# Optimization experiments

Measured on AMD Instinct MI355X. Metric: run time of the kernel, lower is better.

The kernel has to match this reference:

```python
import jax, jax.numpy as jnp
import numpy as np

B = 4096
IN_FEATS = 1024
OUT_FEATS = 1024
NUM_HEADS = 16
NUM_MEMS = 4096
HEAD_DIM = OUT_FEATS // NUM_HEADS
TEMPERATURE = 1.0
EPS = 0.0  # original code uses plain jnp.linalg.norm (no eps)


def setup_inputs() -> dict:
    key = jax.random.key(0)
    k1, k2, k3 = jax.random.split(key, 3)
    x = jax.random.normal(k1, (B, IN_FEATS), dtype=jnp.float32)
    # eqx.nn.Linear stores weight as [out, in]; uniform-like init replaced with normal scaled
    W_q = jax.random.normal(k2, (OUT_FEATS, IN_FEATS), dtype=jnp.float32) * (1.0 / np.sqrt(IN_FEATS))
    memories = jax.random.normal(k3, (NUM_HEADS, NUM_MEMS, HEAD_DIM), dtype=jnp.float32) * 0.02
    return {"x": x, "W_q": W_q, "memories": memories}


def reference(x, W_q, memories):
    # q = query_proj(x): [B, out_feats] -> [B, H, d]
    q = (x @ W_q.T).reshape(B, NUM_HEADS, HEAD_DIM)
    # L2-normalize queries and memories along feature dim
    q_norm = q / jnp.linalg.norm(q, axis=-1, keepdims=True)
    mem_norm = memories / jnp.linalg.norm(memories, axis=-1, keepdims=True)
    # cosine-similarity scores: [B, H, M]
    attn_scores = jnp.einsum('bhd,hmd->bhm', q_norm, mem_norm)
    # soft readout (hard=False branch)
    mem_probs = jax.nn.softmax(attn_scores / TEMPERATURE, axis=-1)
    # weighted combine of normalized memories, scaled by sqrt(head_dim)
    out = jnp.einsum('bhm,hmd->bhd', mem_probs, mem_norm) * jnp.sqrt(HEAD_DIM).astype(x.dtype)
    return out.reshape(B, OUT_FEATS)
```

## Files before the change

kernel.cpp:

```cpp
#include <hip/hip_runtime.h>
#include <stdint.h>

#define B_SZ  4096
#define HEADS 16
#define HD    64
#define M_SZ  4096
#define K_IN  1024
#define SW    72
#define LOG2E 1.44269504088896f

typedef _Float16 f16;
typedef f16  f16x4 __attribute__((ext_vector_type(4)));
typedef f16  f16x8 __attribute__((ext_vector_type(8)));
typedef float f32x4 __attribute__((ext_vector_type(4)));

union U8 { uint4 u4; f16x8 h8; unsigned int ui[4]; unsigned short us[8]; };

__device__ __forceinline__ unsigned short f2h(float f) {
    _Float16 h = (_Float16)f;
    return __builtin_bit_cast(unsigned short, h);
}
__device__ __forceinline__ f16x8 ldsv8(const unsigned short* p) {
    U8 u; u.u4 = *reinterpret_cast<const uint4*>(p); return u.h8;
}

#if __has_builtin(__builtin_amdgcn_exp2f)
#define EXP2F(x) __builtin_amdgcn_exp2f(x)
#else
#define EXP2F(x) __expf((x) * 0.6931471805599453f)
#endif

__device__ __forceinline__ void gload_lds16(const void* g, void* l) {
    __builtin_amdgcn_global_load_lds(
        (const __attribute__((address_space(1))) void*)g,
        (__attribute__((address_space(3))) void*)l, 16, 0, 0);
}

__global__ __launch_bounds__(256) void k_conv(const float* __restrict__ x,
                                              const float* __restrict__ Wq,
                                              unsigned short* __restrict__ xh,
                                              unsigned short* __restrict__ Wh) {
    const int b = blockIdx.x;
    const float* src;
    unsigned short* dst;
    size_t base;
    if (b < 2048) { src = x;  dst = xh; base = (size_t)b * 2048; }
    else          { src = Wq; dst = Wh; base = (size_t)(b - 2048) * 2048; }
    const size_t i = base + (size_t)threadIdx.x * 8;
    float4 f0 = reinterpret_cast<const float4*>(src + i)[0];
    float4 f1 = reinterpret_cast<const float4*>(src + i)[1];
    U8 u;
    u.us[0] = f2h(f0.x); u.us[1] = f2h(f0.y); u.us[2] = f2h(f0.z); u.us[3] = f2h(f0.w);
    u.us[4] = f2h(f1.x); u.us[5] = f2h(f1.y); u.us[6] = f2h(f1.z); u.us[7] = f2h(f1.w);
    *reinterpret_cast<uint4*>(dst + i) = u.u4;
}

__global__ __launch_bounds__(256) void k_prep_mem(const float* __restrict__ mem,
                                                  unsigned short* __restrict__ F) {
    __shared__ float part[64][4];
    __shared__ float scale[64];
    __shared__ unsigned short Tn[64 * SW];

    const int h  = blockIdx.y;
    const int tl = blockIdx.x;
    const int m0 = tl * 64;
    const int tid = threadIdx.x;
    const int r = tid >> 2;
    const int c = tid & 3;

    const float* src = mem + ((size_t)(h * M_SZ + m0 + r)) * HD + c * 16;
    float v[16];
    float ss = 0.f;
#pragma unroll
    for (int i = 0; i < 4; i++) {
        float4 f = reinterpret_cast<const float4*>(src)[i];
        v[4*i+0] = f.x; v[4*i+1] = f.y; v[4*i+2] = f.z; v[4*i+3] = f.w;
        ss += f.x*f.x + f.y*f.y + f.z*f.z + f.w*f.w;
    }
    part[r][c] = ss;
    __syncthreads();
    if (tid < 64) {
        float s = part[tid][0] + part[tid][1] + part[tid][2] + part[tid][3];
        scale[tid] = rsqrtf(s);
    }
    __syncthreads();
    const float sc = scale[r];

    U8 a, b;
#pragma unroll
    for (int i = 0; i < 8; i++) { a.us[i] = f2h(v[i] * sc); b.us[i] = f2h(v[8 + i] * sc); }
    *reinterpret_cast<uint4*>(&Tn[r * SW + c * 16])     = a.u4;
    *reinterpret_cast<uint4*>(&Tn[r * SW + c * 16 + 8]) = b.u4;
    __syncthreads();

    const int w = tid >> 6, lane = tid & 63;
    const int l15 = lane & 15, quad = lane >> 4;
    unsigned short* Fd = F + ((size_t)(h * 64 + tl) * 16) * 512;

#pragma unroll
    for (int i = 0; i < 2; i++) {
        const int ch = w * 2 + i, g = ch >> 1, s = ch & 1;
        const int mp = 32 * (g >> 1) + ((l15 >> 2) * 8) + 4 * (g & 1) + (l15 & 3);
        uint4 vv = *reinterpret_cast<const uint4*>(&Tn[mp * SW + s * 32 + quad * 8]);
        *reinterpret_cast<uint4*>(Fd + ch * 512 + lane * 8) = vv;
    }
#pragma unroll
    for (int i = 0; i < 2; i++) {
        const int c2 = w * 2 + i, p = c2 >> 2, n = c2 & 3;
        U8 u;
#pragma unroll
        for (int j = 0; j < 8; j++)
            u.us[j] = Tn[(32 * p + quad * 8 + j) * SW + n * 16 + l15];
        *reinterpret_cast<uint4*>(Fd + (8 + c2) * 512 + lane * 8) = u.u4;
    }
}

__global__ __launch_bounds__(256, 2) void k_qproj(const unsigned short* __restrict__ xh,
                                                  const unsigned short* __restrict__ Wh,
                                                  unsigned short* __restrict__ qn) {
    __shared__ unsigned short As[128 * SW];
    __shared__ unsigned short Bs[64 * SW];

    const int b0 = blockIdx.x * 128;
    const int n0 = blockIdx.y * 64;
    const int t = threadIdx.x;
    const int w = t >> 6, lane = t & 63;
    const int l15 = lane & 15, quad = lane >> 4;

    f32x4 acc[2][4] = {};

    for (int kb = 0; kb < K_IN; kb += 64) {
        __syncthreads();
        {
            const unsigned short* px = xh + (size_t)(b0 + (t >> 1)) * K_IN + kb + (t & 1) * 32;
            const unsigned short* pw = Wh + (size_t)(n0 + (t >> 2)) * K_IN + kb + (t & 3) * 16;
            uint4 av[4];
#pragma unroll
            for (int i = 0; i < 4; i++) av[i] = reinterpret_cast<const uint4*>(px)[i];
            uint4 bv[2];
#pragma unroll
            for (int i = 0; i < 2; i++) bv[i] = reinterpret_cast<const uint4*>(pw)[i];
#pragma unroll
            for (int i = 0; i < 4; i++)
                *reinterpret_cast<uint4*>(&As[(t >> 1) * SW + (t & 1) * 32 + i * 8]) = av[i];
#pragma unroll
            for (int i = 0; i < 2; i++)
                *reinterpret_cast<uint4*>(&Bs[(t >> 2) * SW + (t & 3) * 16 + i * 8]) = bv[i];
        }
        __syncthreads();

#pragma unroll
        for (int s = 0; s < 2; s++) {
            f16x8 af[2];
#pragma unroll
            for (int qg = 0; qg < 2; qg++)
                af[qg] = ldsv8(&As[(w * 32 + qg * 16 + l15) * SW + s * 32 + quad * 8]);
#pragma unroll
            for (int g = 0; g < 4; g++) {
                f16x8 bf_ = ldsv8(&Bs[(g * 16 + l15) * SW + s * 32 + quad * 8]);
#pragma unroll
                for (int qg = 0; qg < 2; qg++)
                    acc[qg][g] = __builtin_amdgcn_mfma_f32_16x16x32_f16(af[qg], bf_, acc[qg][g], 0, 0, 0);
            }
        }
    }

    __syncthreads();
    unsigned short* Ct = As;
#pragma unroll
    for (int qg = 0; qg < 2; qg++) {
        float ssq[4];
#pragma unroll
        for (int r = 0; r < 4; r++) {
            float s = 0.f;
#pragma unroll
            for (int g = 0; g < 4; g++) s += acc[qg][g][r] * acc[qg][g][r];
            ssq[r] = s;
        }
#pragma unroll
        for (int mask = 1; mask <= 8; mask <<= 1)
#pragma unroll
            for (int r = 0; r < 4; r++) ssq[r] += __shfl_xor(ssq[r], mask, 64);
#pragma unroll
        for (int r = 0; r < 4; r++) {
            float inv = rsqrtf(ssq[r]) * LOG2E;
#pragma unroll
            for (int g = 0; g < 4; g++)
                Ct[(w * 32 + qg * 16 + quad * 4 + r) * SW + g * 16 + l15] = f2h(acc[qg][g][r] * inv);
        }
    }
    __syncthreads();

    const int row = t >> 1, half = (t & 1) * 32;
    unsigned short* dq = qn + (size_t)(b0 + row) * 1024 + n0 + half;
#pragma unroll
    for (int i = 0; i < 4; i++)
        reinterpret_cast<uint4*>(dq)[i] = *reinterpret_cast<const uint4*>(&Ct[row * SW + half + i * 8]);
}

__global__ __launch_bounds__(512, 4) void k_attn(const unsigned short* __restrict__ qn,
                                                 const unsigned short* __restrict__ F,
                                                 float* __restrict__ out) {
    __shared__ unsigned short buf[2][8192];

    const int b = blockIdx.x;
    const int h  = 2 * (b & 7) + (b >> 8);
    const int b0 = ((b >> 3) & 31) * 128;
    const int t = threadIdx.x;
    const int w = t >> 6, lane = t & 63;
    const int l15 = lane & 15, quad = lane >> 4;

    f16x8 qf[2];
#pragma unroll
    for (int s = 0; s < 2; s++) {
        U8 u;
        u.u4 = *reinterpret_cast<const uint4*>(
            qn + (size_t)(b0 + w * 16 + l15) * 1024 + h * 64 + s * 32 + quad * 8);
        qf[s] = u.h8;
    }

    const unsigned short* Fh = F + (size_t)h * 64 * 8192;

    f32x4 accO[4] = {};
    float lsum = 0.f;

    f16x8 puA[2], puB[2];
    f16x8 bwA[8], bwB[8];

#pragma unroll
    for (int i = 0; i < 2; i++) {
        const int ch = w * 2 + i;
        gload_lds16(Fh + ch * 512 + lane * 8, &buf[0][ch * 512]);
    }
    __syncthreads();
    {
        f16x8 am[8];
#pragma unroll
        for (int ch = 0; ch < 8; ch++) am[ch] = ldsv8(&buf[0][ch * 512 + lane * 8]);
#pragma unroll
        for (int ch = 0; ch < 8; ch++) bwA[ch] = ldsv8(&buf[0][(8 + ch) * 512 + lane * 8]);
#pragma unroll
        for (int i = 0; i < 2; i++) {
            const int ch = w * 2 + i;
            gload_lds16(Fh + 8192 + ch * 512 + lane * 8, &buf[1][ch * 512]);
        }
#pragma unroll
        for (int p = 0; p < 2; p++) {
            f32x4 t0 = {0.f,0.f,0.f,0.f}, t1 = {0.f,0.f,0.f,0.f};
            t0 = __builtin_amdgcn_mfma_f32_16x16x32_f16(am[4*p+0], qf[0], t0, 0, 0, 0);
            t0 = __builtin_amdgcn_mfma_f32_16x16x32_f16(am[4*p+1], qf[1], t0, 0, 0, 0);
            t1 = __builtin_amdgcn_mfma_f32_16x16x32_f16(am[4*p+2], qf[0], t1, 0, 0, 0);
            t1 = __builtin_amdgcn_mfma_f32_16x16x32_f16(am[4*p+3], qf[1], t1, 0, 0, 0);
            float p0 = EXP2F(t0[0]), p1 = EXP2F(t0[1]), p2 = EXP2F(t0[2]), p3 = EXP2F(t0[3]);
            float p4 = EXP2F(t1[0]), p5 = EXP2F(t1[1]), p6 = EXP2F(t1[2]), p7 = EXP2F(t1[3]);
            lsum += ((p0 + p1) + (p2 + p3)) + ((p4 + p5) + (p6 + p7));
            U8 pu;
#if __has_builtin(__builtin_amdgcn_cvt_pkrtz)
            pu.ui[0] = __builtin_bit_cast(unsigned int, __builtin_amdgcn_cvt_pkrtz(p0, p1));
            pu.ui[1] = __builtin_bit_cast(unsigned int, __builtin_amdgcn_cvt_pkrtz(p2, p3));
            pu.ui[2] = __builtin_bit_cast(unsigned int, __builtin_amdgcn_cvt_pkrtz(p4, p5));
            pu.ui[3] = __builtin_bit_cast(unsigned int, __builtin_amdgcn_cvt_pkrtz(p6, p7));
#else
            pu.us[0]=f2h(p0); pu.us[1]=f2h(p1); pu.us[2]=f2h(p2); pu.us[3]=f2h(p3);
            pu.us[4]=f2h(p4); pu.us[5]=f2h(p5); pu.us[6]=f2h(p6); pu.us[7]=f2h(p7);
#endif
            puA[p] = pu.h8;
        }
    }

    auto body = [&](int tl, f16x8 (&puC)[2], f16x8 (&bwC)[8],
                            f16x8 (&puN)[2], f16x8 (&bwN)[8]) {
        __syncthreads();
        const unsigned short* lb = buf[(tl + 1) & 1];
        f16x8 amn[8];
#pragma unroll
        for (int ch = 0; ch < 8; ch++) amn[ch] = ldsv8(&lb[ch * 512 + lane * 8]);
#pragma unroll
        for (int ch = 0; ch < 8; ch++) bwN[ch] = ldsv8(&lb[(8 + ch) * 512 + lane * 8]);
        if (tl + 2 < 64) {
            const unsigned short* gsrc = Fh + (size_t)(tl + 2) * 8192;
#pragma unroll
            for (int i = 0; i < 2; i++) {
                const int ch = w * 2 + i;
                gload_lds16(gsrc + ch * 512 + lane * 8, &buf[tl & 1][ch * 512]);
            }
        }

        f32x4 sa[2], sb[2];
        auto expPack = [&](int p) {
            float p0 = EXP2F(sa[p][0]), p1 = EXP2F(sa[p][1]), p2 = EXP2F(sa[p][2]), p3 = EXP2F(sa[p][3]);
            float p4 = EXP2F(sb[p][0]), p5 = EXP2F(sb[p][1]), p6 = EXP2F(sb[p][2]), p7 = EXP2F(sb[p][3]);
            lsum += ((p0 + p1) + (p2 + p3)) + ((p4 + p5) + (p6 + p7));
            U8 pu;
#if __has_builtin(__builtin_amdgcn_cvt_pkrtz)
            pu.ui[0] = __builtin_bit_cast(unsigned int, __builtin_amdgcn_cvt_pkrtz(p0, p1));
            pu.ui[1] = __builtin_bit_cast(unsigned int, __builtin_amdgcn_cvt_pkrtz(p2, p3));
            pu.ui[2] = __builtin_bit_cast(unsigned int, __builtin_amdgcn_cvt_pkrtz(p4, p5));
            pu.ui[3] = __builtin_bit_cast(unsigned int, __builtin_amdgcn_cvt_pkrtz(p6, p7));
#else
            pu.us[0]=f2h(p0); pu.us[1]=f2h(p1); pu.us[2]=f2h(p2); pu.us[3]=f2h(p3);
            pu.us[4]=f2h(p4); pu.us[5]=f2h(p5); pu.us[6]=f2h(p6); pu.us[7]=f2h(p7);
#endif
            puN[p] = pu.h8;
        };

#pragma unroll
        for (int p = 0; p < 2; p++) {
            f32x4 t0 = {0.f,0.f,0.f,0.f}, t1 = {0.f,0.f,0.f,0.f};
            t0 = __builtin_amdgcn_mfma_f32_16x16x32_f16(amn[4*p+0], qf[0], t0, 0, 0, 0);
            t0 = __builtin_amdgcn_mfma_f32_16x16x32_f16(amn[4*p+1], qf[1], t0, 0, 0, 0);
            t1 = __builtin_amdgcn_mfma_f32_16x16x32_f16(amn[4*p+2], qf[0], t1, 0, 0, 0);
            t1 = __builtin_amdgcn_mfma_f32_16x16x32_f16(amn[4*p+3], qf[1], t1, 0, 0, 0);
            sa[p] = t0; sb[p] = t1;
#pragma unroll
            for (int n = 0; n < 4; n++)
                accO[n] = __builtin_amdgcn_mfma_f32_16x16x32_f16(puC[p], bwC[p * 4 + n], accO[n], 0, 0, 0);
            if (p >= 1) expPack(p - 1);
        }
        expPack(1);
    };

    for (int tt = 0; tt < 31; ++tt) {
        body(2 * tt,     puA, bwA, puB, bwB);
        body(2 * tt + 1, puB, bwB, puA, bwA);
    }
    body(62, puA, bwA, puB, bwB);

#pragma unroll
    for (int p = 0; p < 2; p++) {
#pragma unroll
        for (int n = 0; n < 4; n++)
            accO[n] = __builtin_amdgcn_mfma_f32_16x16x32_f16(puB[p], bwB[p * 4 + n], accO[n], 0, 0, 0);
    }

    {
        float s = lsum;
        s += __shfl_xor(s, 16, 64);
        s += __shfl_xor(s, 32, 64);
        float inv = 8.0f / s;
#pragma unroll
        for (int r = 0; r < 4; r++) {
            float iv = __shfl(inv, quad * 4 + r, 64);
            float* po = out + (size_t)(b0 + w * 16 + quad * 4 + r) * 1024 + h * 64;
#pragma unroll
            for (int n = 0; n < 4; n++)
                po[n * 16 + l15] = accO[n][r] * iv;
        }
    }
}

extern "C" void kernel_launch(void* const* d_in, const int* in_sizes, int n_in,
                              void* d_out, int out_size, void* d_ws, size_t ws_size,
                              hipStream_t stream) {
    (void)in_sizes; (void)n_in; (void)out_size; (void)ws_size;
    const float* x   = (const float*)d_in[0];
    const float* Wq  = (const float*)d_in[1];
    const float* mem = (const float*)d_in[2];
    float* out = (float*)d_out;

    unsigned short* qn = (unsigned short*)d_ws;
    unsigned short* F  = qn + (size_t)B_SZ * 1024;
    unsigned short* xh = F  + (size_t)HEADS * 64 * 16 * 512;
    unsigned short* Wh = xh + (size_t)B_SZ * K_IN;

    k_conv    <<<2560, 256, 0, stream>>>(x, Wq, xh, Wh);
    k_prep_mem<<<dim3(64, 16), 256, 0, stream>>>(mem, F);
    k_qproj   <<<dim3(32, 16), 256, 0, stream>>>(xh, Wh, qn);
    k_attn    <<<512, 512, 0, stream>>>(qn, F, out);
}
```

Baseline: 186.3 us.

## Split memory slots across waves and reuse loaded memory tiles for four query groups

The attention kernel now gives each wave four 16-query groups and one quarter of each memory tile, rather than one query group over the whole tile. Each LDS fragment load is therefore reused across four queries, and the memory preprocessing writes a new slot-split layout to match. Partial outputs and softmax sums from the four memory slices are reduced through shared memory in serialized rounds before the final store. In exchange the kernel needs more registers for accumulators, uses a 64KB LDS buffer with occupancy lowered to 2, drops the old software-pipelined exp/PV overlap, and adds a reduction epilogue.

```diff
diff --git a/kernel.cpp b/kernel.cpp
--- a/kernel.cpp
+++ b/kernel.cpp
@@ -95,23 +95,23 @@
 
     const int w = tid >> 6, lane = tid & 63;
     const int l15 = lane & 15, quad = lane >> 4;
-    unsigned short* Fd = F + ((size_t)(h * 64 + tl) * 16) * 512;
-
-#pragma unroll
-    for (int i = 0; i < 2; i++) {
-        const int ch = w * 2 + i, g = ch >> 1, s = ch & 1;
-        const int mp = 32 * (g >> 1) + ((l15 >> 2) * 8) + 4 * (g & 1) + (l15 & 3);
-        uint4 vv = *reinterpret_cast<const uint4*>(&Tn[mp * SW + s * 32 + quad * 8]);
-        *reinterpret_cast<uint4*>(Fd + ch * 512 + lane * 8) = vv;
-    }
-#pragma unroll
-    for (int i = 0; i < 2; i++) {
-        const int c2 = w * 2 + i, p = c2 >> 2, n = c2 & 3;
-        U8 u;
-#pragma unroll
-        for (int j = 0; j < 8; j++)
-            u.us[j] = Tn[(32 * p + quad * 8 + j) * SW + n * 16 + l15];
-        *reinterpret_cast<uint4*>(Fd + (8 + c2) * 512 + lane * 8) = u.u4;
+    const int p  = tl >> 1, hf = tl & 1;
+    const int msl = w;
+    unsigned short* Fd = F + (((size_t)(h * 32 + p) * 4 + msl) * 8) * 512;
+
+#pragma unroll
+    for (int s = 0; s < 2; s++) {
+        uint4 vv = *reinterpret_cast<const uint4*>(&Tn[(msl * 16 + l15) * SW + s * 32 + quad * 8]);
+        *reinterpret_cast<uint4*>(Fd + (hf * 2 + s) * 512 + lane * 8) = vv;
+    }
+#pragma unroll
+    for (int n = 0; n < 4; n++) {
+        unsigned int u0 = Tn[(msl * 16 + quad * 4 + 0) * SW + n * 16 + l15];
+        unsigned int u1 = Tn[(msl * 16 + quad * 4 + 1) * SW + n * 16 + l15];
+        unsigned int u2 = Tn[(msl * 16 + quad * 4 + 2) * SW + n * 16 + l15];
+        unsigned int u3 = Tn[(msl * 16 + quad * 4 + 3) * SW + n * 16 + l15];
+        uint2 uu; uu.x = u0 | (u1 << 16); uu.y = u2 | (u3 << 16);
+        *reinterpret_cast<uint2*>(Fd + (4 + n) * 512 + lane * 8 + hf * 4) = uu;
     }
 }
 
@@ -198,10 +198,11 @@
         reinterpret_cast<uint4*>(dq)[i] = *reinterpret_cast<const uint4*>(&Ct[row * SW + half + i * 8]);
 }
 
-__global__ __launch_bounds__(512, 4) void k_attn(const unsigned short* __restrict__ qn,
+__global__ __launch_bounds__(512, 2) void k_attn(const unsigned short* __restrict__ qn,
                                                  const unsigned short* __restrict__ F,
                                                  float* __restrict__ out) {
-    __shared__ unsigned short buf[2][8192];
+    __shared__ __align__(16) unsigned char smem[65536];
+    unsigned short* bufh = reinterpret_cast<unsigned short*>(smem);
 
     const int b = blockIdx.x;
     const int h  = 2 * (b & 7) + (b >> 8);
@@ -209,51 +210,61 @@
     const int t = threadIdx.x;
     const int w = t >> 6, lane = t & 63;
     const int l15 = lane & 15, quad = lane >> 4;
-
-    f16x8 qf[2];
-#pragma unroll
-    for (int s = 0; s < 2; s++) {
-        U8 u;
-        u.u4 = *reinterpret_cast<const uint4*>(
-            qn + (size_t)(b0 + w * 16 + l15) * 1024 + h * 64 + s * 32 + quad * 8);
-        qf[s] = u.h8;
-    }
-
-    const unsigned short* Fh = F + (size_t)h * 64 * 8192;
-
-    f32x4 accO[4] = {};
-    float lsum = 0.f;
-
-    f16x8 puA[2], puB[2];
-    f16x8 bwA[8], bwB[8];
-
-#pragma unroll
-    for (int i = 0; i < 2; i++) {
-        const int ch = w * 2 + i;
-        gload_lds16(Fh + ch * 512 + lane * 8, &buf[0][ch * 512]);
-    }
-    __syncthreads();
-    {
-        f16x8 am[8];
-#pragma unroll
-        for (int ch = 0; ch < 8; ch++) am[ch] = ldsv8(&buf[0][ch * 512 + lane * 8]);
-#pragma unroll
-        for (int ch = 0; ch < 8; ch++) bwA[ch] = ldsv8(&buf[0][(8 + ch) * 512 + lane * 8]);
-#pragma unroll
-        for (int i = 0; i < 2; i++) {
-            const int ch = w * 2 + i;
-            gload_lds16(Fh + 8192 + ch * 512 + lane * 8, &buf[1][ch * 512]);
-        }
-#pragma unroll
-        for (int p = 0; p < 2; p++) {
-            f32x4 t0 = {0.f,0.f,0.f,0.f}, t1 = {0.f,0.f,0.f,0.f};
-            t0 = __builtin_amdgcn_mfma_f32_16x16x32_f16(am[4*p+0], qf[0], t0, 0, 0, 0);
-            t0 = __builtin_amdgcn_mfma_f32_16x16x32_f16(am[4*p+1], qf[1], t0, 0, 0, 0);
-            t1 = __builtin_amdgcn_mfma_f32_16x16x32_f16(am[4*p+2], qf[0], t1, 0, 0, 0);
-            t1 = __builtin_amdgcn_mfma_f32_16x16x32_f16(am[4*p+3], qf[1], t1, 0, 0, 0);
-            float p0 = EXP2F(t0[0]), p1 = EXP2F(t0[1]), p2 = EXP2F(t0[2]), p3 = EXP2F(t0[3]);
-            float p4 = EXP2F(t1[0]), p5 = EXP2F(t1[1]), p6 = EXP2F(t1[2]), p7 = EXP2F(t1[3]);
-            lsum += ((p0 + p1) + (p2 + p3)) + ((p4 + p5) + (p6 + p7));
+    const int qh = w >> 2, msl = w & 3;
+
+    f16x8 qf[4][2];
+#pragma unroll
+    for (int qg = 0; qg < 4; qg++)
+#pragma unroll
+        for (int s = 0; s < 2; s++) {
+            U8 u;
+            u.u4 = *reinterpret_cast<const uint4*>(
+                qn + (size_t)(b0 + qh * 64 + qg * 16 + l15) * 1024 + h * 64 + s * 32 + quad * 8);
+            qf[qg][s] = u.h8;
+        }
+
+    const unsigned short* Fh = F + (size_t)h * 32 * 16384;
+
+    f32x4 accO[4][4] = {};
+    float lsum[4] = {0.f, 0.f, 0.f, 0.f};
+
+#pragma unroll
+    for (int i = 0; i < 4; i++) {
+        const int cg = w * 4 + i;
+        gload_lds16(Fh + cg * 512 + lane * 8, bufh + cg * 512);
+    }
+
+    for (int p = 0; p < 32; ++p) {
+        __syncthreads();
+        const unsigned short* lb = bufh + (p & 1) * 16384;
+        if (p + 1 < 32) {
+            const unsigned short* gs = Fh + (size_t)(p + 1) * 16384;
+            unsigned short* ls = bufh + ((p + 1) & 1) * 16384;
+#pragma unroll
+            for (int i = 0; i < 4; i++) {
+                const int cg = w * 4 + i;
+                gload_lds16(gs + cg * 512 + lane * 8, ls + cg * 512);
+            }
+        }
+        const unsigned short* mb = lb + msl * 4096;
+        f16x8 a0 = ldsv8(mb + 0 * 512 + lane * 8);
+        f16x8 a1 = ldsv8(mb + 1 * 512 + lane * 8);
+        f16x8 c0 = ldsv8(mb + 2 * 512 + lane * 8);
+        f16x8 c1 = ldsv8(mb + 3 * 512 + lane * 8);
+        f16x8 vf[4];
+#pragma unroll
+        for (int n = 0; n < 4; n++) vf[n] = ldsv8(mb + (4 + n) * 512 + lane * 8);
+
+#pragma unroll
+        for (int qg = 0; qg < 4; qg++) {
+            f32x4 Sa = {0.f,0.f,0.f,0.f}, Sb = {0.f,0.f,0.f,0.f};
+            Sa = __builtin_amdgcn_mfma_f32_16x16x32_f16(a0, qf[qg][0], Sa, 0, 0, 0);
+            Sa = __builtin_amdgcn_mfma_f32_16x16x32_f16(a1, qf[qg][1], Sa, 0, 0, 0);
+            Sb = __builtin_amdgcn_mfma_f32_16x16x32_f16(c0, qf[qg][0], Sb, 0, 0, 0);
+            Sb = __builtin_amdgcn_mfma_f32_16x16x32_f16(c1, qf[qg][1], Sb, 0, 0, 0);
+            float p0 = EXP2F(Sa[0]), p1 = EXP2F(Sa[1]), p2 = EXP2F(Sa[2]), p3 = EXP2F(Sa[3]);
+            float p4 = EXP2F(Sb[0]), p5 = EXP2F(Sb[1]), p6 = EXP2F(Sb[2]), p7 = EXP2F(Sb[3]);
+            lsum[qg] += ((p0 + p1) + (p2 + p3)) + ((p4 + p5) + (p6 + p7));
             U8 pu;
 #if __has_builtin(__builtin_amdgcn_cvt_pkrtz)
             pu.ui[0] = __builtin_bit_cast(unsigned int, __builtin_amdgcn_cvt_pkrtz(p0, p1));
@@ -264,87 +275,64 @@
             pu.us[0]=f2h(p0); pu.us[1]=f2h(p1); pu.us[2]=f2h(p2); pu.us[3]=f2h(p3);
             pu.us[4]=f2h(p4); pu.us[5]=f2h(p5); pu.us[6]=f2h(p6); pu.us[7]=f2h(p7);
 #endif
-            puA[p] = pu.h8;
-        }
-    }
-
-    auto body = [&](int tl, f16x8 (&puC)[2], f16x8 (&bwC)[8],
-                            f16x8 (&puN)[2], f16x8 (&bwN)[8]) {
+            const f16x8 puh = pu.h8;
+#pragma unroll
+            for (int n = 0; n < 4; n++)
+                accO[qg][n] = __builtin_amdgcn_mfma_f32_16x16x32_f16(puh, vf[n], accO[qg][n], 0, 0, 0);
+        }
+    }
+
+    __syncthreads();
+    float* R  = reinterpret_cast<float*>(smem);
+    float* Ls = reinterpret_cast<float*>(smem) + 2 * 64 * 72;
+
+#pragma unroll
+    for (int qg = 0; qg < 4; qg++) {
+        lsum[qg] += __shfl_xor(lsum[qg], 16, 64);
+        lsum[qg] += __shfl_xor(lsum[qg], 32, 64);
+    }
+    if (quad == 0) {
+#pragma unroll
+        for (int qg = 0; qg < 4; qg++) Ls[w * 64 + qg * 16 + l15] = lsum[qg];
+    }
+    float* Rq = R + qh * (64 * 72);
+    for (int rnd = 0; rnd < 4; ++rnd) {
+        if (msl == rnd) {
+            if (rnd == 0) {
+#pragma unroll
+                for (int qg = 0; qg < 4; qg++)
+#pragma unroll
+                    for (int n = 0; n < 4; n++)
+#pragma unroll
+                        for (int r = 0; r < 4; r++)
+                            Rq[(qg * 16 + quad * 4 + r) * 72 + n * 16 + l15] = accO[qg][n][r];
+            } else {
+#pragma unroll
+                for (int qg = 0; qg < 4; qg++)
+#pragma unroll
+                    for (int n = 0; n < 4; n++)
+#pragma unroll
+                        for (int r = 0; r < 4; r++)
+                            Rq[(qg * 16 + quad * 4 + r) * 72 + n * 16 + l15] += accO[qg][n][r];
+            }
+        }
         __syncthreads();
-        const unsigned short* lb = buf[(tl + 1) & 1];
-        f16x8 amn[8];
-#pragma unroll
-        for (int ch = 0; ch < 8; ch++) amn[ch] = ldsv8(&lb[ch * 512 + lane * 8]);
-#pragma unroll
-        for (int ch = 0; ch < 8; ch++) bwN[ch] = ldsv8(&lb[(8 + ch) * 512 + lane * 8]);
-        if (tl + 2 < 64) {
-            const unsigned short* gsrc = Fh + (size_t)(tl + 2) * 8192;
-#pragma unroll
-            for (int i = 0; i < 2; i++) {
-                const int ch = w * 2 + i;
-                gload_lds16(gsrc + ch * 512 + lane * 8, &buf[tl & 1][ch * 512]);
-            }
-        }
-
-        f32x4 sa[2], sb[2];
-        auto expPack = [&](int p) {
-            float p0 = EXP2F(sa[p][0]), p1 = EXP2F(sa[p][1]), p2 = EXP2F(sa[p][2]), p3 = EXP2F(sa[p][3]);
-            float p4 = EXP2F(sb[p][0]), p5 = EXP2F(sb[p][1]), p6 = EXP2F(sb[p][2]), p7 = EXP2F(sb[p][3]);
-            lsum += ((p0 + p1) + (p2 + p3)) + ((p4 + p5) + (p6 + p7));
-            U8 pu;
-#if __has_builtin(__builtin_amdgcn_cvt_pkrtz)
-            pu.ui[0] = __builtin_bit_cast(unsigned int, __builtin_amdgcn_cvt_pkrtz(p0, p1));
-            pu.ui[1] = __builtin_bit_cast(unsigned int, __builtin_amdgcn_cvt_pkrtz(p2, p3));
-            pu.ui[2] = __builtin_bit_cast(unsigned int, __builtin_amdgcn_cvt_pkrtz(p4, p5));
-            pu.ui[3] = __builtin_bit_cast(unsigned int, __builtin_amdgcn_cvt_pkrtz(p6, p7));
-#else
-            pu.us[0]=f2h(p0); pu.us[1]=f2h(p1); pu.us[2]=f2h(p2); pu.us[3]=f2h(p3);
-            pu.us[4]=f2h(p4); pu.us[5]=f2h(p5); pu.us[6]=f2h(p6); pu.us[7]=f2h(p7);
-#endif
-            puN[p] = pu.h8;
-        };
-
-#pragma unroll
-        for (int p = 0; p < 2; p++) {
-            f32x4 t0 = {0.f,0.f,0.f,0.f}, t1 = {0.f,0.f,0.f,0.f};
-            t0 = __builtin_amdgcn_mfma_f32_16x16x32_f16(amn[4*p+0], qf[0], t0, 0, 0, 0);
-            t0 = __builtin_amdgcn_mfma_f32_16x16x32_f16(amn[4*p+1], qf[1], t0, 0, 0, 0);
-            t1 = __builtin_amdgcn_mfma_f32_16x16x32_f16(amn[4*p+2], qf[0], t1, 0, 0, 0);
-            t1 = __builtin_amdgcn_mfma_f32_16x16x32_f16(amn[4*p+3], qf[1], t1, 0, 0, 0);
-            sa[p] = t0; sb[p] = t1;
-#pragma unroll
-            for (int n = 0; n < 4; n++)
-                accO[n] = __builtin_amdgcn_mfma_f32_16x16x32_f16(puC[p], bwC[p * 4 + n], accO[n], 0, 0, 0);
-            if (p >= 1) expPack(p - 1);
-        }
-        expPack(1);
-    };
-
-    for (int tt = 0; tt < 31; ++tt) {
-        body(2 * tt,     puA, bwA, puB, bwB);
-        body(2 * tt + 1, puB, bwB, puA, bwA);
-    }
-    body(62, puA, bwA, puB, bwB);
-
-#pragma unroll
-    for (int p = 0; p < 2; p++) {
-#pragma unroll
-        for (int n = 0; n < 4; n++)
-            accO[n] = __builtin_amdgcn_mfma_f32_16x16x32_f16(puB[p], bwB[p * 4 + n], accO[n], 0, 0, 0);
     }
 
     {
-        float s = lsum;
-        s += __shfl_xor(s, 16, 64);
-        s += __shfl_xor(s, 32, 64);
-        float inv = 8.0f / s;
-#pragma unroll
-        for (int r = 0; r < 4; r++) {
-            float iv = __shfl(inv, quad * 4 + r, 64);
-            float* po = out + (size_t)(b0 + w * 16 + quad * 4 + r) * 1024 + h * 64;
-#pragma unroll
-            for (int n = 0; n < 4; n++)
-                po[n * 16 + l15] = accO[n][r] * iv;
+        const int q   = t >> 2;
+        const int dq  = t & 3;
+        const int qh2 = q >> 6, ql = q & 63;
+        const float lt = Ls[(qh2 * 4 + 0) * 64 + ql] + Ls[(qh2 * 4 + 1) * 64 + ql]
+                       + Ls[(qh2 * 4 + 2) * 64 + ql] + Ls[(qh2 * 4 + 3) * 64 + ql];
+        const float inv = 8.0f / lt;
+        const float* Rr = R + qh2 * (64 * 72) + ql * 72 + dq * 16;
+        float* po = out + (size_t)(b0 + q) * 1024 + h * 64 + dq * 16;
+#pragma unroll
+        for (int j = 0; j < 4; j++) {
+            f32x4 v = *reinterpret_cast<const f32x4*>(Rr + j * 4);
+            v = v * inv;
+            *reinterpret_cast<f32x4*>(po + j * 4) = v;
         }
     }
 }
```

Result: slower. 210.6 us (+13.0%).
